# Performance work log

Measured on AMD Instinct MI355X. Metric: run time of the kernel, lower is better.

Reference implementation:

```python
import jax, jax.numpy as jnp
import numpy as np

NUM_SCALE_LAYERS = [16, 8, 8]
B, H, N = 32, 512, 64
NUM_PROPS = 2080


def _pool_specs():
    # (kernel, stride) per layer, matching the torch ModuleList construction
    specs = []
    for scale_idx, num_layer in enumerate(NUM_SCALE_LAYERS):
        first = (1, 1) if scale_idx == 0 else (3, 2)
        specs.append([first] + [(2, 1)] * (num_layer - 1))
    return specs


def _maxpool1d(x, k, s):
    # x: [B, H, L] -> valid max pool along last axis
    return jax.lax.reduce_window(x, -jnp.inf, jax.lax.max,
                                 (1, 1, k), (1, 1, s), 'VALID')


def setup_inputs() -> dict:
    key = jax.random.key(0)
    kx, ks, ke = jax.random.split(key, 3)
    x = jax.random.normal(kx, (B, H, N), dtype=jnp.float32)
    starts = jax.random.randint(ks, (NUM_PROPS,), 0, N)          # props[:,0] in [0, N)
    ends = jax.random.randint(ke, (NUM_PROPS,), 1, N + 1)        # props[:,1] in [1, N]
    props = jnp.stack([starts, ends], axis=1).astype(jnp.int64)
    return {"x": x, "props": props}


def reference(x, props):
    batch_size, hidden_size, ori_num_clips = x.shape
    ori_map_h = jnp.zeros((batch_size, hidden_size, ori_num_clips, ori_num_clips), x.dtype)
    ori_map_mask = jnp.zeros((batch_size, 1, ori_num_clips, ori_num_clips), x.dtype)
    acum_layers = 0
    stride = 1
    for scale_layers in _pool_specs():
        for i, (k, s) in enumerate(scale_layers):
            stride = stride * s
            x = _maxpool1d(x, k, s)
            # static (trace-time) diagonal index lists, exactly as the torch code
            s_idxs = np.arange(0, ori_num_clips - acum_layers - i * stride, stride)
            e_idxs = s_idxs + acum_layers + i * stride
            ori_map_h = ori_map_h.at[:, :, s_idxs, e_idxs].set(x)
            ori_map_mask = ori_map_mask.at[:, :, s_idxs, e_idxs].set(1.0)
        acum_layers += stride * (len(scale_layers) + 1)
    props_h = ori_map_h[:, :, props[:, 0], props[:, 1] - 1]      # [B, H, P]
    ori_map_mask = ori_map_mask.at[:, :, props[:, 0], props[:, 1] - 1].set(1.0)
    return props_h.swapaxes(1, 2), ori_map_h, ori_map_mask
```

## Files before the change

### kernel.cpp

```cpp
#include <hip/hip_runtime.h>
#include <math.h>

#define PB 32
#define PH 512
#define PN 64
#define PP 2080

#define OFF_MAP  ((size_t)PB * PP * PH)
#define OFF_MASK (OFF_MAP + (size_t)PB * PH * PN * PN)

__device__ __forceinline__ bool pair_valid(int s, int e) {
    int d = e - s;
    if (d < 0) return false;
    if (d <= 15) return true;
    if (d <= 31) return (d & 1) && !(s & 1);
    return d >= 35 && ((d & 3) == 3) && !(s & 3);
}

__global__ __launch_bounds__(64) void map_kernel(const float* __restrict__ x,
                                                 float* __restrict__ out) {
    const int bid  = blockIdx.x;
    const int lane = threadIdx.x;
    __shared__ float sx[PN];

    sx[lane] = x[(size_t)bid * PN + lane];
    __syncthreads();

    const int h = bid & (PH - 1);
    const int b = bid >> 9;
    float* mrow = out + OFF_MAP + (size_t)bid * (PN * PN);
    float* krow = out + OFF_MASK + (size_t)b * (PN * PN);
    const bool write_mask = (h == 0);

    float M = -INFINITY;
#pragma unroll 1
    for (int s = PN - 1; s >= 0; --s) {
        const float v = sx[s];
        if (s <= lane) M = fmaxf(M, v);
        const bool good = (lane >= s) && pair_valid(s, lane);
        mrow[s * PN + lane] = good ? M : 0.0f;
        if (write_mask) krow[s * PN + lane] = good ? 1.0f : 0.0f;
    }
}

#define P_CHUNKS 13
#define PC (PP / P_CHUNKS)
__global__ __launch_bounds__(64) void props_kernel(const float* __restrict__ x,
                                                   const int* __restrict__ props,
                                                   float* __restrict__ out) {
    const int b    = blockIdx.z;
    const int h0   = blockIdx.y * 64;
    const int p0   = blockIdx.x * PC;
    const int lane = threadIdx.x;

    __shared__ float sx[PN * 65];

    const float* xb = x + ((size_t)b * PH + h0) * PN;
#pragma unroll 4
    for (int i = 0; i < 64; ++i) {
        sx[lane * 65 + i] = xb[i * PN + lane];
    }
    __syncthreads();

    float* op = out + (size_t)b * PP * PH + h0;
#pragma unroll 1
    for (int p = p0; p < p0 + PC; ++p) {
        const int s  = props[2 * p];
        const int e1 = props[2 * p + 1] - 1;
        float m = 0.0f;
        if (e1 >= s && pair_valid(s, e1)) {
            m = -INFINITY;
            for (int n = s; n <= e1; ++n)
                m = fmaxf(m, sx[n * 65 + lane]);
        }
        op[(size_t)p * PH + lane] = m;
    }
}

__global__ void mask_props_kernel(const int* __restrict__ props,
                                  float* __restrict__ out) {
    const int idx = blockIdx.x * blockDim.x + threadIdx.x;
    if (idx >= PB * PP) return;
    const int b = idx / PP;
    const int p = idx - b * PP;
    const int s  = props[2 * p];
    const int e1 = props[2 * p + 1] - 1;
    out[OFF_MASK + (size_t)b * (PN * PN) + s * PN + e1] = 1.0f;
}

extern "C" void kernel_launch(void* const* d_in, const int* in_sizes, int n_in,
                              void* d_out, int out_size, void* d_ws, size_t ws_size,
                              hipStream_t stream) {
    const float* x = (const float*)d_in[0];
    const int* props = (const int*)d_in[1];
    float* out = (float*)d_out;

    map_kernel<<<PB * PH, 64, 0, stream>>>(x, out);
    dim3 g2(P_CHUNKS, PH / 64, PB);
    props_kernel<<<g2, 64, 0, stream>>>(x, props, out);
    mask_props_kernel<<<(PB * PP + 255) / 256, 256, 0, stream>>>(props, out);
}
```

Baseline: 505.7 us.

## Use sparse-table range max with vectorized stores for map and props kernels

Both kernels now build a log-level sparse table of sliding-window maxima in shared memory, so every (s,e) range max becomes the max of two table lookups instead of a serial scan. The map kernel handles 8 rows per 256-thread block and writes float4 stores, with lookup indices computed once per thread. The mask base moves to its own kernel rather than being written by the h==0 blocks. The aim is to cut per-element serial loops and widen the stores to the 268MB map output, in exchange for extra shared memory and barriers.

```diff
diff --git a/kernel.cpp b/kernel.cpp
--- a/kernel.cpp
+++ b/kernel.cpp
@@ -17,64 +17,140 @@
     return d >= 35 && ((d & 3) == 3) && !(s & 3);
 }
 
-__global__ __launch_bounds__(64) void map_kernel(const float* __restrict__ x,
-                                                 float* __restrict__ out) {
-    const int bid  = blockIdx.x;
-    const int lane = threadIdx.x;
-    __shared__ float sx[PN];
+#define K1_ROWS 8
+#define K1_RS 385
 
-    sx[lane] = x[(size_t)bid * PN + lane];
+__global__ __launch_bounds__(256) void map_kernel(const float* __restrict__ x,
+                                                  float* __restrict__ out) {
+    __shared__ float L[K1_ROWS * K1_RS];
+    const int tid = threadIdx.x;
+
+    int a1[16], a2[16];
+#pragma unroll
+    for (int j = 0; j < 4; ++j) {
+#pragma unroll
+        for (int q = 0; q < 4; ++q) {
+            const int idx = j * 4 + q;
+            const int lin = j * 1024 + tid * 4 + q;
+            const int s = lin >> 6, e = lin & 63;
+            const bool good = pair_valid(s, e);
+            const int du = (e - s) + 1;
+            const int k = good ? min(31 - __clz(du), 5) : 0;
+            a1[idx] = good ? k * 64 + s : 384;
+            a2[idx] = good ? k * 64 + (e + 1 - (1 << k)) : 384;
+        }
+    }
+
+    const size_t rowBase = (size_t)blockIdx.x * K1_ROWS;
+#pragma unroll
+    for (int i = tid; i < K1_ROWS * 64; i += 256) {
+        const int r = i >> 6, c = i & 63;
+        L[r * K1_RS + c] = x[rowBase * 64 + i];
+    }
+    if (tid < K1_ROWS) L[tid * K1_RS + 384] = 0.0f;
     __syncthreads();
 
-    const int h = bid & (PH - 1);
-    const int b = bid >> 9;
-    float* mrow = out + OFF_MAP + (size_t)bid * (PN * PN);
-    float* krow = out + OFF_MASK + (size_t)b * (PN * PN);
-    const bool write_mask = (h == 0);
+#pragma unroll
+    for (int k = 1; k <= 5; ++k) {
+        const int off = 1 << (k - 1);
+#pragma unroll
+        for (int i = tid; i < K1_ROWS * 64; i += 256) {
+            const int r = i >> 6, c = i & 63;
+            const float* Lp = L + r * K1_RS + (k - 1) * 64;
+            L[r * K1_RS + k * 64 + c] = fmaxf(Lp[c], Lp[min(c + off, 63)]);
+        }
+        __syncthreads();
+    }
 
-    float M = -INFINITY;
 #pragma unroll 1
-    for (int s = PN - 1; s >= 0; --s) {
-        const float v = sx[s];
-        if (s <= lane) M = fmaxf(M, v);
-        const bool good = (lane >= s) && pair_valid(s, lane);
-        mrow[s * PN + lane] = good ? M : 0.0f;
-        if (write_mask) krow[s * PN + lane] = good ? 1.0f : 0.0f;
+    for (int r = 0; r < K1_ROWS; ++r) {
+        const float* Lr = L + r * K1_RS;
+        float4* orow = (float4*)(out + OFF_MAP + (rowBase + r) * 4096);
+#pragma unroll
+        for (int j = 0; j < 4; ++j) {
+            float4 v;
+            v.x = fmaxf(Lr[a1[j * 4 + 0]], Lr[a2[j * 4 + 0]]);
+            v.y = fmaxf(Lr[a1[j * 4 + 1]], Lr[a2[j * 4 + 1]]);
+            v.z = fmaxf(Lr[a1[j * 4 + 2]], Lr[a2[j * 4 + 2]]);
+            v.w = fmaxf(Lr[a1[j * 4 + 3]], Lr[a2[j * 4 + 3]]);
+            orow[j * 256 + tid] = v;
+        }
     }
 }
 
-#define P_CHUNKS 13
-#define PC (PP / P_CHUNKS)
-__global__ __launch_bounds__(64) void props_kernel(const float* __restrict__ x,
-                                                   const int* __restrict__ props,
-                                                   float* __restrict__ out) {
-    const int b    = blockIdx.z;
-    const int h0   = blockIdx.y * 64;
-    const int p0   = blockIdx.x * PC;
-    const int lane = threadIdx.x;
+#define K2_LVL 2112
+#define K2_ZROW (6 * K2_LVL)
+#define K2_PA (K2_ZROW + 33)
+#define K2_PC 160
+#define K2_CHUNKS 13
 
-    __shared__ float sx[PN * 65];
+__global__ __launch_bounds__(256) void props_kernel(const float* __restrict__ x,
+                                                    const int* __restrict__ props,
+                                                    float* __restrict__ out) {
+    __shared__ float Lf[K2_PA + 2 * K2_PC];
+    int* Li = (int*)Lf;
+
+    const int tid = threadIdx.x;
+    const int b  = blockIdx.z;
+    const int h0 = blockIdx.y * 32;
+    const int p0 = blockIdx.x * K2_PC;
 
     const float* xb = x + ((size_t)b * PH + h0) * PN;
-#pragma unroll 4
-    for (int i = 0; i < 64; ++i) {
-        sx[lane * 65 + i] = xb[i * PN + lane];
+#pragma unroll
+    for (int i = tid; i < 32 * 64; i += 256) {
+        const int h = i >> 6, n = i & 63;
+        Lf[n * 33 + h] = xb[i];
+    }
+    if (tid < 33) Lf[K2_ZROW + tid] = 0.0f;
+
+    if (tid < K2_PC) {
+        const int p  = p0 + tid;
+        const int s  = props[2 * p];
+        const int e1 = props[2 * p + 1] - 1;
+        const bool good = pair_valid(s, e1);
+        const int k = good ? min(31 - __clz(e1 - s + 1), 5) : 0;
+        Li[K2_PA + 2 * tid]     = good ? k * K2_LVL + s * 33 : K2_ZROW;
+        Li[K2_PA + 2 * tid + 1] = good ? k * K2_LVL + (e1 + 1 - (1 << k)) * 33 : K2_ZROW;
     }
     __syncthreads();
 
-    float* op = out + (size_t)b * PP * PH + h0;
 #pragma unroll 1
-    for (int p = p0; p < p0 + PC; ++p) {
-        const int s  = props[2 * p];
-        const int e1 = props[2 * p + 1] - 1;
-        float m = 0.0f;
-        if (e1 >= s && pair_valid(s, e1)) {
-            m = -INFINITY;
-            for (int n = s; n <= e1; ++n)
-                m = fmaxf(m, sx[n * 65 + lane]);
+    for (int k = 1; k <= 5; ++k) {
+        const int off = 1 << (k - 1);
+#pragma unroll
+        for (int i = tid; i < 64 * 32; i += 256) {
+            const int n = i >> 5, h = i & 31;
+            const float* Lp = Lf + (k - 1) * K2_LVL;
+            Lf[k * K2_LVL + n * 33 + h] = fmaxf(Lp[n * 33 + h], Lp[min(n + off, 63) * 33 + h]);
         }
-        op[(size_t)p * PH + lane] = m;
+        __syncthreads();
     }
+
+    const int wave = tid >> 6;
+    const int sub  = (tid >> 5) & 1;
+    const int h    = tid & 31;
+    float* ob = out + (size_t)b * PP * PH + h0 + h;
+#pragma unroll 2
+    for (int i = 0; i < K2_PC / 8; ++i) {
+        const int idx = i * 8 + wave * 2 + sub;
+        const int a1 = Li[K2_PA + 2 * idx];
+        const int a2 = Li[K2_PA + 2 * idx + 1];
+        const float v = fmaxf(Lf[a1 + h], Lf[a2 + h]);
+        ob[(size_t)(p0 + idx) * PH] = v;
+    }
+}
+
+__global__ void mask_base_kernel(float* __restrict__ out) {
+    const int gid = blockIdx.x * blockDim.x + threadIdx.x;
+    const int l4 = (gid & 1023) * 4;
+    float4 v;
+    float* vv = (float*)&v;
+#pragma unroll
+    for (int q = 0; q < 4; ++q) {
+        const int lin = l4 + q;
+        vv[q] = pair_valid(lin >> 6, lin & 63) ? 1.0f : 0.0f;
+    }
+    ((float4*)(out + OFF_MASK))[gid] = v;
 }
 
 __global__ void mask_props_kernel(const int* __restrict__ props,
@@ -95,8 +171,11 @@
     const int* props = (const int*)d_in[1];
     float* out = (float*)d_out;
 
-    map_kernel<<<PB * PH, 64, 0, stream>>>(x, out);
-    dim3 g2(P_CHUNKS, PH / 64, PB);
-    props_kernel<<<g2, 64, 0, stream>>>(x, props, out);
+    map_kernel<<<(PB * PH) / K1_ROWS, 256, 0, stream>>>(x, out);
+
+    dim3 g2(K2_CHUNKS, PH / 32, PB);
+    props_kernel<<<g2, 256, 0, stream>>>(x, props, out);
+
+    mask_base_kernel<<<(PB * 1024) / 256, 256, 0, stream>>>(out);
     mask_props_kernel<<<(PB * PP + 255) / 256, 256, 0, stream>>>(props, out);
 }
```

New measurement: 485.8 us. 1.04x faster.
